# Performance work log

Hardware: AMD Instinct MI355X
Metric: run time of the kernel (lower is better)

## Reference

```python
import jax, jax.numpy as jnp
import numpy as np

D, H, S, L = 512, 8, 4, 2
HD = D // H          # 64 head dim
F = 4 * D            # 2048 FFN hidden
EPS = 1e-5


def setup_inputs() -> dict:
    key = jax.random.key(0)
    ks = jax.random.split(key, 26)
    B = 16384
    w = 0.02
    inp = {
        'text_pattern':   jax.random.normal(ks[0], (B, D), jnp.float32),
        'text_semantic':  jax.random.normal(ks[1], (B, D), jnp.float32),
        'image_pattern':  jax.random.normal(ks[2], (B, D), jnp.float32),
        'image_semantic': jax.random.normal(ks[3], (B, D), jnp.float32),
        # per-(layer, stream) attention projections, stacked [L,S,...]
        'Wq': jax.random.normal(ks[4], (L, S, D, D), jnp.float32) * w,
        'bq': jnp.zeros((L, S, D), jnp.float32),
        'Wk': jax.random.normal(ks[5], (L, S, D, D), jnp.float32) * w,
        'bk': jnp.zeros((L, S, D), jnp.float32),
        'Wv': jax.random.normal(ks[6], (L, S, D, D), jnp.float32) * w,
        'bv': jnp.zeros((L, S, D), jnp.float32),
        'Wo': jax.random.normal(ks[7], (L, S, D, D), jnp.float32) * w,
        'bo': jnp.zeros((L, S, D), jnp.float32),
        'ln_g': jnp.ones((L, S, D), jnp.float32),
        'ln_b': jnp.zeros((L, S, D), jnp.float32),
        'W1': jax.random.normal(ks[8], (L, S, D, F), jnp.float32) * w,
        'b1': jnp.zeros((L, S, F), jnp.float32),
        'W2': jax.random.normal(ks[9], (L, S, F, D), jnp.float32) * w,
        'b2': jnp.zeros((L, S, D), jnp.float32),
        # final fusion MLP: 4*D -> 2*D -> D
        'Wf1': jax.random.normal(ks[10], (S * D, 2 * D), jnp.float32) * w,
        'bf1': jnp.zeros((2 * D,), jnp.float32),
        'Wf2': jax.random.normal(ks[11], (2 * D, D), jnp.float32) * w,
        'bf2': jnp.zeros((D,), jnp.float32),
    }
    return inp


def _layer_norm(x, g, b):
    # x: [B,S,D], g/b: [S,D]; normalize over last dim
    mu = jnp.mean(x, axis=-1, keepdims=True)
    var = jnp.mean(jnp.square(x - mu), axis=-1, keepdims=True)
    return (x - mu) * jax.lax.rsqrt(var + EPS) * g + b


def reference(text_pattern, text_semantic, image_pattern, image_semantic,
              Wq, bq, Wk, bk, Wv, bv, Wo, bo, ln_g, ln_b,
              W1, b1, W2, b2, Wf1, bf1, Wf2, bf2):
    # streams stacked: [B, S=4, D]; each stream's query_len is 1, keys are all 4 streams
    x = jnp.stack([text_pattern, text_semantic, image_pattern, image_semantic], axis=1)
    B = x.shape[0]
    attn0 = None
    for l in range(L):
        # per-stream query projection of its own token: [B,S,D]
        q = jnp.einsum('bsd,sde->bse', x, Wq[l]) + bq[l]
        # per-stream K/V projections of ALL streams: [B,S(query-stream),K(key-pos),D]
        k = jnp.einsum('bkd,sde->bske', x, Wk[l]) + bk[l][:, None, :]
        v = jnp.einsum('bkd,sde->bske', x, Wv[l]) + bv[l][:, None, :]
        qh = q.reshape(B, S, H, HD)
        kh = k.reshape(B, S, S, H, HD)
        vh = v.reshape(B, S, S, H, HD)
        scores = jnp.einsum('bshe,bskhe->bshk', qh, kh) / (HD ** 0.5)  # [B,S,H,K]
        w = jax.nn.softmax(scores, axis=-1)
        ctx = jnp.einsum('bshk,bskhe->bshe', w, vh).reshape(B, S, D)
        attn_out = jnp.einsum('bsd,sde->bse', ctx, Wo[l]) + bo[l]
        if l == 0:
            attn0 = w  # [B,S,H,K]: layer-0 attention weights per stream
        h = _layer_norm(x + attn_out, ln_g[l], ln_b[l])
        ffn = jnp.einsum('bsf,sfd->bsd',
                         jax.nn.relu(jnp.einsum('bsd,sdf->bsf', h, W1[l]) + b1[l]),
                         W2[l]) + b2[l]
        x = h + ffn
    concat = x.reshape(B, S * D)
    fused = jax.nn.relu(concat @ Wf1 + bf1) @ Wf2 + bf2  # [B, D]
    return fused, attn0
```

## Files before the change

kernel.cpp:

```cpp
#include <hip/hip_runtime.h>
#include <stdint.h>

typedef unsigned short u16;
typedef __bf16 bf16x8 __attribute__((ext_vector_type(8)));
typedef float f32x4 __attribute__((ext_vector_type(4)));

constexpr int NB = 16384;
constexpr int DM = 512;
constexpr int NS = 4;
constexpr int FH = 2048;
constexpr int XW = NS * DM;
constexpr float EPSL = 1e-5f;

__device__ __forceinline__ float bf2f(u16 u) { return __uint_as_float(((uint32_t)u) << 16); }
__device__ __forceinline__ u16 f2bf(float f) {
  uint32_t u = __float_as_uint(f);
  u += 0x7fffu + ((u >> 16) & 1u);
  return (u16)(u >> 16);
}
__device__ __forceinline__ void unpack8(uint4 p, float* f) {
  f[0] = __uint_as_float(p.x << 16); f[1] = __uint_as_float(p.x & 0xffff0000u);
  f[2] = __uint_as_float(p.y << 16); f[3] = __uint_as_float(p.y & 0xffff0000u);
  f[4] = __uint_as_float(p.z << 16); f[5] = __uint_as_float(p.z & 0xffff0000u);
  f[6] = __uint_as_float(p.w << 16); f[7] = __uint_as_float(p.w & 0xffff0000u);
}
__device__ __forceinline__ uint4 pack8(const float* f) {
  uint4 r;
  r.x = (uint32_t)f2bf(f[0]) | ((uint32_t)f2bf(f[1]) << 16);
  r.y = (uint32_t)f2bf(f[2]) | ((uint32_t)f2bf(f[3]) << 16);
  r.z = (uint32_t)f2bf(f[4]) | ((uint32_t)f2bf(f[5]) << 16);
  r.w = (uint32_t)f2bf(f[6]) | ((uint32_t)f2bf(f[7]) << 16);
  return r;
}
__device__ __forceinline__ uint32_t cvtpk(float lo, float hi) {
  uint32_t d;
  asm("v_cvt_pk_bf16_f32 %0, %1, %2" : "=v"(d) : "v"(lo), "v"(hi));
  return d;
}
__device__ __forceinline__ void gl_lds16(const void* g, void* l) {
  __builtin_amdgcn_global_load_lds((const __attribute__((address_space(1))) void*)g,
                                   (__attribute__((address_space(3))) void*)l, 16, 0, 0);
}

__device__ __forceinline__ void remap(int& bx, int& by, int& bz) {
  const int gx = gridDim.x, gy = gridDim.y;
  const int fl = (blockIdx.z * gy + blockIdx.y) * gx + blockIdx.x;
  const int xcd = fl & 7;
  const int t = fl >> 3;
  const int bw = gx >> 3;
  bx = xcd * bw + t % bw;
  const int u = t / bw;
  by = u % gy;
  bz = u / gy;
}

__device__ __forceinline__ void gemm_cv(
    const u16* __restrict__ A, int lda,
    const u16* __restrict__ Bt, int K,
    u16* As, u16* Bs, f32x4 (&acc)[4][4], int bx, int by)
{
  const int tid = threadIdx.x;
  const int ln = tid & 63;
  const int w  = tid >> 6;
  const int wm = w >> 1, wn = w & 1;
  const int m0 = bx * 128;
  const int n0 = by * 128;
  const int grow = ln >> 2;
  const int gcol = ((ln & 3) ^ ((ln >> 3) & 3)) * 8;
  const u16* Ab = A  + (size_t)(m0 + w * 32 + grow) * lda + gcol;
  const u16* Bb = Bt + (size_t)(n0 + w * 32 + grow) * K   + gcol;

  auto stage = [&](int buf, int k0) {
#pragma unroll
    for (int i = 0; i < 2; ++i) {
      gl_lds16(Ab + (size_t)i * 16 * lda + k0, &As[buf * 4096 + (w * 32 + i * 16) * 32]);
      gl_lds16(Bb + (size_t)i * 16 * K   + k0, &Bs[buf * 4096 + (w * 32 + i * 16) * 32]);
    }
  };

  __syncthreads();
  const int nt = K >> 5;
  stage(0, 0);
  if (nt > 1) {
    stage(1, 32);
    asm volatile("s_waitcnt vmcnt(4)" ::: "memory");
  } else {
    asm volatile("s_waitcnt vmcnt(0)" ::: "memory");
  }
  __builtin_amdgcn_s_barrier();
  asm volatile("" ::: "memory");

  const int rx = ((ln & 15) >> 1) & 3;
  const int qb = ln >> 4;
  const int cb = (qb ^ rx) * 8;
  int cur = 0, nxt2 = 2;
  for (int t = 0; t < nt; ++t) {
    bf16x8 af[4], bfv[4];
#pragma unroll
    for (int m = 0; m < 4; ++m) {
      af[m]  = *(const bf16x8*)&As[cur * 4096 + (wm * 64 + m * 16 + (ln & 15)) * 32 + cb];
      bfv[m] = *(const bf16x8*)&Bs[cur * 4096 + (wn * 64 + m * 16 + (ln & 15)) * 32 + cb];
    }
#pragma unroll
    for (int m = 0; m < 4; ++m)
#pragma unroll
      for (int n = 0; n < 4; ++n)
        acc[m][n] = __builtin_amdgcn_mfma_f32_16x16x32_bf16(af[m], bfv[n], acc[m][n], 0, 0, 0);
    if (t + 2 < nt) {
      stage(nxt2, (t + 2) * 32);
      asm volatile("s_waitcnt vmcnt(4)" ::: "memory");
      __builtin_amdgcn_s_barrier();
      asm volatile("" ::: "memory");
    } else if (t + 1 < nt) {
      asm volatile("s_waitcnt vmcnt(0)" ::: "memory");
      __builtin_amdgcn_s_barrier();
      asm volatile("" ::: "memory");
    }
    cur = cur + 1;  if (cur == 3)  cur = 0;
    nxt2 = nxt2 + 1; if (nxt2 == 3) nxt2 = 0;
  }
  asm volatile("" ::: "memory");
}

template<bool RELU, bool RESID, bool OUTF32>
__global__ __launch_bounds__(256) void k_gemm(
    const u16* __restrict__ A, int lda, long aZ,
    const u16* __restrict__ Bt, long bZ,
    const float* __restrict__ bias, long biasZ,
    const u16* __restrict__ Rsd, int ldr, long rZ,
    void* __restrict__ Cp, int ldc, long cZ, int K)
{
  int bx, by, bz; remap(bx, by, bz);
  A += (long)bz * aZ; Bt += (long)bz * bZ; bias += (long)bz * biasZ;
  __shared__ alignas(16) u16 As[3 * 4096];
  __shared__ alignas(16) u16 Bs[3 * 4096];
  f32x4 acc[4][4] = {};
  gemm_cv(A, lda, Bt, K, As, Bs, acc, bx, by);
  const int ln = threadIdx.x & 63;
  const int w = threadIdx.x >> 6;
  const int wm = w >> 1, wn = w & 1;
  const int m0 = bx * 128, n0 = by * 128;
#pragma unroll
  for (int n = 0; n < 4; ++n) {
    const int gc = n0 + wn * 64 + n * 16 + (ln & 15);
    const float bv = bias[gc];
#pragma unroll
    for (int m = 0; m < 4; ++m) {
#pragma unroll
      for (int j = 0; j < 4; ++j) {
        const int gr = m0 + wm * 64 + m * 16 + (ln >> 4) * 4 + j;
        float v = acc[m][n][j] + bv;
        if constexpr (RESID) v += bf2f(Rsd[(long)bz * rZ + (size_t)gr * ldr + gc]);
        if constexpr (RELU)  v = v > 0.f ? v : 0.f;
        if constexpr (OUTF32) ((float*)Cp)[(long)bz * cZ + (size_t)gr * ldc + gc] = v;
        else                  ((u16*)Cp)[(long)bz * cZ + (size_t)gr * ldc + gc] = f2bf(v);
      }
    }
  }
}

__global__ __launch_bounds__(256) void k_kdot(
    const u16* __restrict__ xcat, const u16* __restrict__ WkT_l,
    const u16* __restrict__ Qb, float* __restrict__ wbuf)
{
  int bx, by, kp; remap(bx, by, kp);
  __shared__ alignas(16) u16 As[3 * 4096];
  __shared__ alignas(16) u16 Bs[3 * 4096];
  f32x4 acc[4][4] = {};
  gemm_cv(xcat + kp * DM, XW, WkT_l, DM, As, Bs, acc, bx, by);
  const int ln = threadIdx.x & 63;
  const int w = threadIdx.x >> 6;
  const int wm = w >> 1, wn = w & 1;
  const int m0 = bx * 128, n0 = by * 128;
  const int colbase = n0 + wn * 64;
  const int s = colbase >> 9;
  const int h = (colbase >> 6) & 7;
  float p[4][4];
#pragma unroll
  for (int m = 0; m < 4; ++m)
#pragma unroll
    for (int j = 0; j < 4; ++j) p[m][j] = 0.f;
#pragma unroll
  for (int n = 0; n < 4; ++n) {
    const int qc = (colbase & 511) + n * 16 + (ln & 15);
#pragma unroll
    for (int m = 0; m < 4; ++m) {
#pragma unroll
      for (int j = 0; j < 4; ++j) {
        const int gr = m0 + wm * 64 + m * 16 + (ln >> 4) * 4 + j;
        p[m][j] += acc[m][n][j] * bf2f(Qb[((size_t)s * NB + gr) * DM + qc]);
      }
    }
  }
#pragma unroll
  for (int m = 0; m < 4; ++m)
#pragma unroll
    for (int j = 0; j < 4; ++j) {
      float v = p[m][j];
      v += __shfl_xor(v, 1, 64);
      v += __shfl_xor(v, 2, 64);
      v += __shfl_xor(v, 4, 64);
      v += __shfl_xor(v, 8, 64);
      p[m][j] = v;
    }
  if ((ln & 15) == 0) {
#pragma unroll
    for (int m = 0; m < 4; ++m)
#pragma unroll
      for (int j = 0; j < 4; ++j) {
        const int gr = m0 + wm * 64 + m * 16 + (ln >> 4) * 4 + j;
        wbuf[(((size_t)s * NB + gr) * 8 + h) * 4 + kp] = p[m][j] * 0.125f;
      }
  }
}

__global__ __launch_bounds__(256) void k_gemmvm(
    const u16* __restrict__ xcat, const u16* __restrict__ WvT_l,
    const float* __restrict__ bv_l, const float* __restrict__ wbuf,
    u16* __restrict__ ctxc)
{
  int bx, by, bz; remap(bx, by, bz); (void)bz;
  __shared__ alignas(16) u16 Am[2 * 8192];
  __shared__ alignas(16) u16 Bsh[2 * 4096];
  const int tid = threadIdx.x;
  const int ln = tid & 63;
  const int w  = tid >> 6;
  const int wm = w >> 1, wn = w & 1;
  const int m0 = bx * 128;
  const int n0 = by * 128;
  const int s  = n0 >> 9;
  const int h0 = (n0 >> 6) & 7;
  const int lr = ln & 15;
  const int kq = (ln >> 4) * 8;
  const u16* Abase = xcat  + (size_t)(m0 + w * 32 + lr) * XW + kq;
  const u16* Bbase = WvT_l + (size_t)(n0 + w * 32 + lr) * DM + kq;

  float4 wg[2][2];
#pragma unroll
  for (int i = 0; i < 2; ++i) {
    const int r = m0 + (w * 2 + i) * 16 + lr;
#pragma unroll
    for (int j = 0; j < 2; ++j)
      wg[i][j] = *(const float4*)&wbuf[(((size_t)s * NB + r) * 8 + h0 + j) * 4];
  }

  uint4 ar[2][4];
  auto loadA = [&](int k0) {
#pragma unroll
    for (int i = 0; i < 2; ++i)
#pragma unroll
      for (int kp = 0; kp < 4; ++kp)
        ar[i][kp] = *(const uint4*)(Abase + (size_t)i * 16 * XW + kp * DM + k0);
  };
  auto loadB = [&](int buf, int k0) {
#pragma unroll
    for (int i = 0; i < 2; ++i)
      gl_lds16(Bbase + (size_t)i * 16 * DM + k0,
               &Bsh[buf * 4096 + (w * 2 + i) * 512 + ln * 8]);
  };
  auto mixwrite = [&](int buf) {
#pragma unroll
    for (int i = 0; i < 2; ++i) {
      float x[4][8];
#pragma unroll
      for (int kp = 0; kp < 4; ++kp) unpack8(ar[i][kp], x[kp]);
#pragma unroll
      for (int j = 0; j < 2; ++j) {
        const float4 g = wg[i][j];
        float o[8];
#pragma unroll
        for (int e = 0; e < 8; ++e)
          o[e] = g.x * x[0][e] + g.y * x[1][e] + g.z * x[2][e] + g.w * x[3][e];
        uint4 pk;
        pk.x = cvtpk(o[0], o[1]); pk.y = cvtpk(o[2], o[3]);
        pk.z = cvtpk(o[4], o[5]); pk.w = cvtpk(o[6], o[7]);
        *(uint4*)&Am[buf * 8192 + ((j * 8) + (w * 2 + i)) * 512 + ln * 8] = pk;
      }
    }
  };

  f32x4 acc[4][4] = {};
  const int nt = DM / 32;

  loadA(0); loadB(0, 0);
  asm volatile("s_waitcnt vmcnt(0)" ::: "memory");
  mixwrite(0);
  asm volatile("s_waitcnt lgkmcnt(0)" ::: "memory");
  __builtin_amdgcn_s_barrier();
  asm volatile("" ::: "memory");

  int cbuf = 0;
  for (int t = 0; t < nt; ++t) {
    if (t + 1 < nt) { loadA((t + 1) * 32); loadB(cbuf ^ 1, (t + 1) * 32); }
    bf16x8 af[4], bfv[4];
#pragma unroll
    for (int m = 0; m < 4; ++m)
      af[m] = *(const bf16x8*)&Am[cbuf * 8192 + (wn * 8 + wm * 4 + m) * 512 + ln * 8];
#pragma unroll
    for (int n = 0; n < 4; ++n)
      bfv[n] = *(const bf16x8*)&Bsh[cbuf * 4096 + (wn * 4 + n) * 512 + ln * 8];
#pragma unroll
    for (int m = 0; m < 4; ++m)
#pragma unroll
      for (int n = 0; n < 4; ++n)
        acc[m][n] = __builtin_amdgcn_mfma_f32_16x16x32_bf16(af[m], bfv[n], acc[m][n], 0, 0, 0);
    if (t + 1 < nt) {
      asm volatile("s_waitcnt vmcnt(0)" ::: "memory");
      mixwrite(cbuf ^ 1);
      asm volatile("s_waitcnt lgkmcnt(0)" ::: "memory");
      __builtin_amdgcn_s_barrier();
      asm volatile("" ::: "memory");
      cbuf ^= 1;
    }
  }

#pragma unroll
  for (int nf = 0; nf < 4; ++nf) {
    const int gc = n0 + wn * 64 + nf * 16 + (ln & 15);
    const float bvv = bv_l[gc];
#pragma unroll
    for (int mf = 0; mf < 4; ++mf) {
#pragma unroll
      for (int j = 0; j < 4; ++j) {
        const int gr = m0 + wm * 64 + mf * 16 + (ln >> 4) * 4 + j;
        ctxc[(size_t)gr * XW + gc] = f2bf(acc[mf][nf][j] + bvv);
      }
    }
  }
}

__global__ __launch_bounds__(256) void k_softmax(
    float* __restrict__ wbuf, float* __restrict__ a0)
{
  const int t = blockIdx.x * 256 + threadIdx.x;
  float4 v = ((const float4*)wbuf)[t];
  const float mx = fmaxf(fmaxf(v.x, v.y), fmaxf(v.z, v.w));
  float4 e;
  e.x = __expf(v.x - mx); e.y = __expf(v.y - mx);
  e.z = __expf(v.z - mx); e.w = __expf(v.w - mx);
  const float inv = 1.f / (e.x + e.y + e.z + e.w);
  e.x *= inv; e.y *= inv; e.z *= inv; e.w *= inv;
  ((float4*)wbuf)[t] = e;
  if (a0 != nullptr) {
    const int s = t >> 17, b = (t >> 3) & (NB - 1), h = t & 7;
    ((float4*)a0)[((size_t)b * NS + s) * 8 + h] = e;
  }
}

__global__ __launch_bounds__(256) void k_ln(
    u16* __restrict__ xcat, const float* __restrict__ g, const float* __restrict__ bb)
{
  const int ln = threadIdx.x & 63;
  const int row = blockIdx.x * 4 + (threadIdx.x >> 6);
  const int b = row >> 2, s = row & 3;
  u16* p = xcat + (size_t)b * XW + s * DM;
  float v[8];
  { uint4 t = ((const uint4*)p)[ln]; unpack8(t, v); }
  float sum = 0.f;
#pragma unroll
  for (int j = 0; j < 8; ++j) sum += v[j];
#pragma unroll
  for (int off = 1; off < 64; off <<= 1) sum += __shfl_xor(sum, off, 64);
  const float mu = sum * (1.f / DM);
  float s2 = 0.f;
#pragma unroll
  for (int j = 0; j < 8; ++j) { float d = v[j] - mu; s2 += d * d; }
#pragma unroll
  for (int off = 1; off < 64; off <<= 1) s2 += __shfl_xor(s2, off, 64);
  const float rs = rsqrtf(s2 * (1.f / DM) + EPSL);
  const int e0 = s * DM + ln * 8;
  float o[8];
#pragma unroll
  for (int j = 0; j < 8; ++j) o[j] = (v[j] - mu) * rs * g[e0 + j] + bb[e0 + j];
  ((uint4*)p)[ln] = pack8(o);
}

__global__ void k_pack(const float* __restrict__ t0, const float* __restrict__ t1,
                       const float* __restrict__ t2, const float* __restrict__ t3,
                       u16* __restrict__ xcat)
{
  const int total = NB * XW / 8;
  for (int t = blockIdx.x * blockDim.x + threadIdx.x; t < total; t += gridDim.x * blockDim.x) {
    const int b = t >> 8;
    const int r = t & 255;
    const int s = r >> 6;
    const int d0 = (r & 63) * 8;
    const float* p = (s == 0) ? t0 : (s == 1) ? t1 : (s == 2) ? t2 : t3;
    float f[8];
#pragma unroll
    for (int j = 0; j < 8; ++j) f[j] = p[(size_t)b * DM + d0 + j];
    ((uint4*)xcat)[t] = pack8(f);
  }
}

__global__ __launch_bounds__(256) void k_tcvt(
    const float* __restrict__ src, u16* __restrict__ dst, int R, int C)
{
  __shared__ float tl[32][33];
  const int cx = blockIdx.x * 32, ry = blockIdx.y * 32;
  const size_t base = (size_t)blockIdx.z * R * C;
  const int lx = threadIdx.x & 31, ly = threadIdx.x >> 5;
#pragma unroll
  for (int i = 0; i < 32; i += 8)
    tl[ly + i][lx] = src[base + (size_t)(ry + ly + i) * C + cx + lx];
  __syncthreads();
#pragma unroll
  for (int i = 0; i < 32; i += 8)
    dst[base + (size_t)(cx + ly + i) * R + ry + lx] = f2bf(tl[lx][ly + i]);
}

extern "C" void kernel_launch(void* const* d_in, const int* in_sizes, int n_in,
                              void* d_out, int out_size, void* d_ws, size_t ws_size,
                              hipStream_t stream)
{
  (void)in_sizes; (void)n_in; (void)out_size;
  const float* t0  = (const float*)d_in[0];
  const float* t1  = (const float*)d_in[1];
  const float* t2  = (const float*)d_in[2];
  const float* t3  = (const float*)d_in[3];
  const float* Wq  = (const float*)d_in[4];
  const float* bq  = (const float*)d_in[5];
  const float* Wk  = (const float*)d_in[6];
  const float* Wv  = (const float*)d_in[8];
  const float* bv  = (const float*)d_in[9];
  const float* Wo  = (const float*)d_in[10];
  const float* bo  = (const float*)d_in[11];
  const float* lng = (const float*)d_in[12];
  const float* lnb = (const float*)d_in[13];
  const float* W1  = (const float*)d_in[14];
  const float* b1  = (const float*)d_in[15];
  const float* W2  = (const float*)d_in[16];
  const float* b2  = (const float*)d_in[17];
  const float* Wf1 = (const float*)d_in[18];
  const float* bf1 = (const float*)d_in[19];
  const float* Wf2 = (const float*)d_in[20];
  const float* bf2 = (const float*)d_in[21];

  size_t off = 0;
  char* ws = (char*)d_ws;
  auto take = [&](size_t n) { char* p = ws + off; off += (n + 255) & ~(size_t)255; return p; };
  u16* WqT  = (u16*)take(8ull * DM * DM * 2);
  u16* WkT  = (u16*)take(8ull * DM * DM * 2);
  u16* WvT  = (u16*)take(8ull * DM * DM * 2);
  u16* WoT  = (u16*)take(8ull * DM * DM * 2);
  u16* W1T  = (u16*)take(8ull * DM * FH * 2);
  u16* W2T  = (u16*)take(8ull * FH * DM * 2);
  u16* Wf1T = (u16*)take((size_t)XW * 1024 * 2);
  u16* Wf2T = (u16*)take((size_t)1024 * DM * 2);
  u16* xcat = (u16*)take((size_t)NB * XW * 2);
  char* U1  = take((size_t)NB * XW * 2);
  float* wbuf = (float*)take(4ull * NB * 8 * 4 * 4);
  const size_t base_needed = off;

  u16* ffnb = nullptr;
  long RCH = 0;
  if (base_needed + 4ull * NB * FH * 2 <= ws_size) {
    ffnb = (u16*)take(4ull * NB * FH * 2);  RCH = NB;
  } else if (base_needed + 2ull * NB * FH * 2 <= ws_size) {
    ffnb = (u16*)take(2ull * NB * FH * 2);  RCH = NB / 2;
  }

  u16* Qb   = (u16*)U1;
  u16* ctxc = (u16*)U1;
  u16* ffn1 = (u16*)U1;
  u16* y1   = (u16*)U1;
  float* attn0 = (float*)d_out + (size_t)NB * DM;

  if (base_needed > ws_size) return;

  k_tcvt<<<dim3(16, 16, 8), dim3(256), 0, stream>>>(Wq, WqT, DM, DM);
  k_tcvt<<<dim3(16, 16, 8), dim3(256), 0, stream>>>(Wk, WkT, DM, DM);
  k_tcvt<<<dim3(16, 16, 8), dim3(256), 0, stream>>>(Wv, WvT, DM, DM);
  k_tcvt<<<dim3(16, 16, 8), dim3(256), 0, stream>>>(Wo, WoT, DM, DM);
  k_tcvt<<<dim3(64, 16, 8), dim3(256), 0, stream>>>(W1, W1T, DM, FH);
  k_tcvt<<<dim3(16, 64, 8), dim3(256), 0, stream>>>(W2, W2T, FH, DM);
  k_tcvt<<<dim3(32, 64, 1), dim3(256), 0, stream>>>(Wf1, Wf1T, XW, 1024);
  k_tcvt<<<dim3(16, 32, 1), dim3(256), 0, stream>>>(Wf2, Wf2T, 1024, DM);
  k_pack<<<dim3(2048), dim3(256), 0, stream>>>(t0, t1, t2, t3, xcat);

  const long WSQ = (long)DM * DM;
  for (int ly = 0; ly < 2; ++ly) {
    const u16* WqT_l = WqT + (size_t)ly * 4 * WSQ;
    const u16* WkT_l = WkT + (size_t)ly * 4 * WSQ;
    const u16* WvT_l = WvT + (size_t)ly * 4 * WSQ;
    const u16* WoT_l = WoT + (size_t)ly * 4 * WSQ;
    k_gemm<false, false, false><<<dim3(128, 4, 4), dim3(256), 0, stream>>>(
        xcat, XW, DM, WqT_l, WSQ, bq + (size_t)ly * XW, DM,
        nullptr, 0, 0, Qb, DM, (long)NB * DM, DM);
    k_kdot<<<dim3(128, 16, 4), dim3(256), 0, stream>>>(xcat, WkT_l, Qb, wbuf);
    k_softmax<<<dim3(4 * NB * 8 / 256), dim3(256), 0, stream>>>(
        wbuf, (ly == 0) ? attn0 : (float*)nullptr);
    k_gemmvm<<<dim3(128, 16), dim3(256), 0, stream>>>(
        xcat, WvT_l, bv + (size_t)ly * XW, wbuf, ctxc);
    k_gemm<false, true, false><<<dim3(128, 4, 4), dim3(256), 0, stream>>>(
        ctxc, XW, DM, WoT_l, WSQ, bo + (size_t)ly * XW, DM,
        xcat, XW, DM, xcat, XW, DM, DM);
    k_ln<<<dim3(NB), dim3(256), 0, stream>>>(xcat, lng + ly * XW, lnb + ly * XW);
    if (RCH > 0) {
      for (long c0 = 0; c0 < NB; c0 += RCH) {
        k_gemm<true, false, false><<<dim3((int)(RCH / 128), 16, 4), dim3(256), 0, stream>>>(
            xcat + c0 * XW, XW, DM,
            W1T + (size_t)ly * 4 * DM * FH, (long)DM * FH,
            b1 + (size_t)ly * 4 * FH, FH,
            nullptr, 0, 0, ffnb, FH, (long)RCH * FH, DM);
        k_gemm<false, true, false><<<dim3((int)(RCH / 128), 4, 4), dim3(256), 0, stream>>>(
            ffnb, FH, (long)RCH * FH,
            W2T + (size_t)ly * 4 * FH * DM, (long)FH * DM,
            b2 + (size_t)ly * 4 * DM, DM,
            xcat + c0 * XW, XW, DM, xcat + c0 * XW, XW, DM, FH);
      }
    } else {
      for (int s = 0; s < NS; ++s) {
        const size_t wsl = (size_t)(ly * 4 + s);
        k_gemm<true, false, false><<<dim3(128, 16, 1), dim3(256), 0, stream>>>(
            xcat + s * DM, XW, 0, W1T + wsl * (size_t)DM * FH, 0, b1 + wsl * FH, 0,
            nullptr, 0, 0, ffn1, FH, 0, DM);
        k_gemm<false, true, false><<<dim3(128, 4, 1), dim3(256), 0, stream>>>(
            ffn1, FH, 0, W2T + wsl * (size_t)FH * DM, 0, b2 + wsl * DM, 0,
            xcat + s * DM, XW, 0, xcat + s * DM, XW, 0, FH);
      }
    }
  }
  k_gemm<true, false, false><<<dim3(128, 8, 1), dim3(256), 0, stream>>>(
      xcat, XW, 0, Wf1T, 0, bf1, 0, nullptr, 0, 0, y1, 1024, 0, XW);
  k_gemm<false, false, true><<<dim3(128, 4, 1), dim3(256), 0, stream>>>(
      y1, 1024, 0, Wf2T, 0, bf2, 0, nullptr, 0, 0, d_out, DM, 0, 1024);
}
```

Before: 2.233 ms.

## Deepen V-projection pipeline with two register stages and register-staged B loads

Rewrites the mixed-V GEMM main loop to keep two sets of prefetch registers, so global loads for tile t+2 are issued before tile t+1 is consumed. It uses partial vmcnt waits instead of full drains. B tiles now travel through registers and are written to LDS together with the mixed A tile, replacing the direct global-to-LDS load. The aim is to hide global load latency behind the MFMA work, at the cost of more VGPRs and possible occupancy loss.

```diff
diff --git a/kernel.cpp b/kernel.cpp
--- a/kernel.cpp
+++ b/kernel.cpp
@@ -244,75 +244,97 @@
       wg[i][j] = *(const float4*)&wbuf[(((size_t)s * NB + r) * 8 + h0 + j) * 4];
   }
 
-  uint4 ar[2][4];
-  auto loadA = [&](int k0) {
-#pragma unroll
-    for (int i = 0; i < 2; ++i)
-#pragma unroll
-      for (int kp = 0; kp < 4; ++kp)
-        ar[i][kp] = *(const uint4*)(Abase + (size_t)i * 16 * XW + kp * DM + k0);
-  };
-  auto loadB = [&](int buf, int k0) {
-#pragma unroll
-    for (int i = 0; i < 2; ++i)
-      gl_lds16(Bbase + (size_t)i * 16 * DM + k0,
-               &Bsh[buf * 4096 + (w * 2 + i) * 512 + ln * 8]);
-  };
-  auto mixwrite = [&](int buf) {
-#pragma unroll
-    for (int i = 0; i < 2; ++i) {
-      float x[4][8];
-#pragma unroll
-      for (int kp = 0; kp < 4; ++kp) unpack8(ar[i][kp], x[kp]);
-#pragma unroll
-      for (int j = 0; j < 2; ++j) {
-        const float4 g = wg[i][j];
-        float o[8];
-#pragma unroll
-        for (int e = 0; e < 8; ++e)
-          o[e] = g.x * x[0][e] + g.y * x[1][e] + g.z * x[2][e] + g.w * x[3][e];
-        uint4 pk;
-        pk.x = cvtpk(o[0], o[1]); pk.y = cvtpk(o[2], o[3]);
-        pk.z = cvtpk(o[4], o[5]); pk.w = cvtpk(o[6], o[7]);
-        *(uint4*)&Am[buf * 8192 + ((j * 8) + (w * 2 + i)) * 512 + ln * 8] = pk;
-      }
-    }
-  };
+  uint4 arA0[2][4], arA1[2][4];
+  uint4 brB0[2],    brB1[2];
+
+#define LOADT(AR, BR, k0)                                                     \
+  {                                                                           \
+    _Pragma("unroll")                                                         \
+    for (int i = 0; i < 2; ++i) {                                             \
+      _Pragma("unroll")                                                       \
+      for (int kp = 0; kp < 4; ++kp)                                          \
+        AR[i][kp] = *(const uint4*)(Abase + (size_t)i * 16 * XW + kp * DM + (k0)); \
+      BR[i] = *(const uint4*)(Bbase + (size_t)i * 16 * DM + (k0));            \
+    }                                                                         \
+    asm volatile("" ::: "memory");                                            \
+  }
+
+#define MIXW(AR, BR, buf)                                                     \
+  {                                                                           \
+    _Pragma("unroll")                                                         \
+    for (int i = 0; i < 2; ++i) {                                             \
+      float x[4][8];                                                          \
+      _Pragma("unroll")                                                       \
+      for (int kp = 0; kp < 4; ++kp) unpack8(AR[i][kp], x[kp]);               \
+      _Pragma("unroll")                                                       \
+      for (int j = 0; j < 2; ++j) {                                           \
+        const float4 g = wg[i][j];                                            \
+        float o[8];                                                           \
+        _Pragma("unroll")                                                     \
+        for (int e = 0; e < 8; ++e)                                           \
+          o[e] = g.x * x[0][e] + g.y * x[1][e] + g.z * x[2][e] + g.w * x[3][e]; \
+        uint4 pk;                                                             \
+        pk.x = cvtpk(o[0], o[1]); pk.y = cvtpk(o[2], o[3]);                   \
+        pk.z = cvtpk(o[4], o[5]); pk.w = cvtpk(o[6], o[7]);                   \
+        *(uint4*)&Am[(buf) * 8192 + ((j * 8) + (w * 2 + i)) * 512 + ln * 8] = pk; \
+      }                                                                       \
+      *(uint4*)&Bsh[(buf) * 4096 + (w * 2 + i) * 512 + ln * 8] = BR[i];       \
+    }                                                                         \
+  }
+
+#define MFMAS(buf)                                                            \
+  {                                                                           \
+    bf16x8 af[4], bfv[4];                                                     \
+    _Pragma("unroll")                                                         \
+    for (int m = 0; m < 4; ++m)                                               \
+      af[m] = *(const bf16x8*)&Am[(buf) * 8192 + (wn * 8 + wm * 4 + m) * 512 + ln * 8]; \
+    _Pragma("unroll")                                                         \
+    for (int n = 0; n < 4; ++n)                                               \
+      bfv[n] = *(const bf16x8*)&Bsh[(buf) * 4096 + (wn * 4 + n) * 512 + ln * 8]; \
+    _Pragma("unroll")                                                         \
+    for (int m = 0; m < 4; ++m)                                               \
+      _Pragma("unroll")                                                       \
+      for (int n = 0; n < 4; ++n)                                             \
+        acc[m][n] = __builtin_amdgcn_mfma_f32_16x16x32_bf16(af[m], bfv[n], acc[m][n], 0, 0, 0); \
+  }
 
   f32x4 acc[4][4] = {};
-  const int nt = DM / 32;
-
-  loadA(0); loadB(0, 0);
+  constexpr int nt = DM / 32;
+
+  LOADT(arA0, brB0, 0);
   asm volatile("s_waitcnt vmcnt(0)" ::: "memory");
-  mixwrite(0);
+  MIXW(arA0, brB0, 0);
+  LOADT(arA1, brB1, 32);
   asm volatile("s_waitcnt lgkmcnt(0)" ::: "memory");
   __builtin_amdgcn_s_barrier();
   asm volatile("" ::: "memory");
 
-  int cbuf = 0;
-  for (int t = 0; t < nt; ++t) {
-    if (t + 1 < nt) { loadA((t + 1) * 32); loadB(cbuf ^ 1, (t + 1) * 32); }
-    bf16x8 af[4], bfv[4];
-#pragma unroll
-    for (int m = 0; m < 4; ++m)
-      af[m] = *(const bf16x8*)&Am[cbuf * 8192 + (wn * 8 + wm * 4 + m) * 512 + ln * 8];
-#pragma unroll
-    for (int n = 0; n < 4; ++n)
-      bfv[n] = *(const bf16x8*)&Bsh[cbuf * 4096 + (wn * 4 + n) * 512 + ln * 8];
-#pragma unroll
-    for (int m = 0; m < 4; ++m)
-#pragma unroll
-      for (int n = 0; n < 4; ++n)
-        acc[m][n] = __builtin_amdgcn_mfma_f32_16x16x32_bf16(af[m], bfv[n], acc[m][n], 0, 0, 0);
-    if (t + 1 < nt) {
-      asm volatile("s_waitcnt vmcnt(0)" ::: "memory");
-      mixwrite(cbuf ^ 1);
+#pragma unroll
+  for (int t = 0; t < nt; t += 2) {
+    if (t + 2 < nt) LOADT(arA0, brB0, (t + 2) * 32);
+    MFMAS(0);
+    {
+      if (t + 2 < nt) { asm volatile("s_waitcnt vmcnt(10)" ::: "memory"); }
+      else            { asm volatile("s_waitcnt vmcnt(0)"  ::: "memory"); }
+      MIXW(arA1, brB1, 1);
       asm volatile("s_waitcnt lgkmcnt(0)" ::: "memory");
       __builtin_amdgcn_s_barrier();
       asm volatile("" ::: "memory");
-      cbuf ^= 1;
-    }
-  }
+    }
+    if (t + 3 < nt) LOADT(arA1, brB1, (t + 3) * 32);
+    MFMAS(1);
+    if (t + 2 < nt) {
+      if (t + 3 < nt) { asm volatile("s_waitcnt vmcnt(10)" ::: "memory"); }
+      else            { asm volatile("s_waitcnt vmcnt(0)"  ::: "memory"); }
+      MIXW(arA0, brB0, 0);
+      asm volatile("s_waitcnt lgkmcnt(0)" ::: "memory");
+      __builtin_amdgcn_s_barrier();
+      asm volatile("" ::: "memory");
+    }
+  }
+#undef LOADT
+#undef MIXW
+#undef MFMAS
 
 #pragma unroll
   for (int nf = 0; nf < 4; ++nf) {
```

New measurement: 2.227 ms. About the same (-0.3%).
